# Kernel tuning notes

Measured on AMD Instinct MI355X. Metric: run time of the kernel, lower is better.

## Reference

```python
import jax, jax.numpy as jnp
import numpy as np

IN_DIM = 512
QK_DIM = IN_DIM // 8

def setup_inputs() -> dict:
    key = jax.random.key(0)
    ks = jax.random.split(key, 8)
    x = jax.random.normal(ks[0], (8, IN_DIM, 64, 64), dtype=jnp.float32)
    s_in = 1.0 / np.sqrt(IN_DIM)
    Wq = jax.random.normal(ks[1], (QK_DIM, IN_DIM), dtype=jnp.float32) * s_in
    bq = jnp.zeros((QK_DIM,), dtype=jnp.float32)
    Wk = jax.random.normal(ks[2], (QK_DIM, IN_DIM), dtype=jnp.float32) * s_in
    bk = jnp.zeros((QK_DIM,), dtype=jnp.float32)
    Wv = jax.random.normal(ks[3], (IN_DIM, IN_DIM), dtype=jnp.float32) * s_in
    bv = jnp.zeros((IN_DIM,), dtype=jnp.float32)
    # gamma initialized to zero in the module; use small nonzero so output depends on attention path
    gamma = jnp.array([0.1], dtype=jnp.float32)
    return {"x": x, "Wq": Wq, "bq": bq, "Wk": Wk, "bk": bk, "Wv": Wv, "bv": bv, "gamma": gamma}

def reference(x, Wq, bq, Wk, bk, Wv, bv, gamma):
    b, c, h, w = x.shape
    n = h * w
    xf = x.reshape(b, c, n)  # (b, C, N)
    # 1x1 convs are per-pixel linear maps over channels
    q = jnp.einsum('oc,bcn->bno', Wq, xf) + bq  # (b, N, Cq)
    k = jnp.einsum('oc,bcn->bon', Wk, xf) + bk[None, :, None]  # (b, Cq, N)
    energy = jnp.einsum('bno,bom->bnm', q, k)  # (b, N, N), no scaling (as in source)
    attention = jax.nn.softmax(energy, axis=-1)
    v = jnp.einsum('oc,bcn->bon', Wv, xf) + bv[None, :, None]  # (b, C, N)
    # out[b,c,i] = sum_j v[b,c,j] * attention[b,i,j]  (bmm with attention^T)
    out = jnp.einsum('bcj,bij->bci', v, attention).reshape(b, c, h, w)
    return gamma[0] * out + x
```

## Files before the change

### kernel.cpp

```cpp
#include <hip/hip_runtime.h>
#include <hip/hip_bf16.h>
#include <cstddef>

#define BB 8
#define CC 512
#define NN 4096
#define CQ 64
#define MQ 64
#define NJ 64

typedef short bf16x8 __attribute__((ext_vector_type(8)));
typedef float f32x4  __attribute__((ext_vector_type(4)));

static __device__ __forceinline__ unsigned bf16_bits(float f){
  unsigned u = __float_as_uint(f);
  u += 0x7fffu + ((u >> 16) & 1u);
  return u >> 16;
}
static __device__ __forceinline__ unsigned pack2bf(float lo, float hi){
  return bf16_bits(lo) | (bf16_bits(hi) << 16);
}

__global__ __launch_bounds__(256) void cvt_w_kernel(
    const float* __restrict__ Wq, const float* __restrict__ Wk,
    const float* __restrict__ Wv,
    short* __restrict__ Wqkbf, short* __restrict__ Wvbf){
  const int i = blockIdx.x*256 + threadIdx.x;
  if (i < CQ*CC){
    Wqkbf[i]         = (short)bf16_bits(Wq[i]);
    Wqkbf[CQ*CC + i] = (short)bf16_bits(Wk[i]);
  }
  Wvbf[i] = (short)bf16_bits(Wv[i]);
}

__global__ __launch_bounds__(256) void cvt_x_kernel(
    const float* __restrict__ x, short* __restrict__ xT){
  __shared__ float lds[64*67];
  const int tid = threadIdx.x;
  const int n0 = blockIdx.x*64, c0 = blockIdx.y*64, b = blockIdx.z;
  const int nl = tid & 63, cw = tid >> 6;
  const float* xp = x + ((size_t)b*CC + c0)*NN + n0;
#pragma unroll
  for (int i=0;i<16;++i){
    const int cl = cw*16 + i;
    lds[nl*67 + cl] = xp[(size_t)cl*NN + nl];
  }
  __syncthreads();
  short* xTp = xT + ((size_t)b*NN + n0)*CC + c0;
#pragma unroll
  for (int p=0;p<2;++p){
    const int nl2 = (tid>>3) + p*32;
    const int c8 = (tid&7)*8;
    const float* r = &lds[nl2*67 + c8];
    uint4 v;
    v.x = pack2bf(r[0], r[1]);
    v.y = pack2bf(r[2], r[3]);
    v.z = pack2bf(r[4], r[5]);
    v.w = pack2bf(r[6], r[7]);
    *(uint4*)&xTp[(size_t)nl2*CC + c8] = v;
  }
}

__global__ __launch_bounds__(256) void proj_qk_mfma(
    const short* __restrict__ xT, const short* __restrict__ Wqkbf,
    const float* __restrict__ bq, const float* __restrict__ bk,
    short* __restrict__ Qbf, short* __restrict__ Kbf){
  const int tid  = threadIdx.x;
  const int lane = tid & 63;
  const int w    = tid >> 6;
  const int iq   = lane & 15;
  const int q    = lane >> 4;
  const int b    = blockIdx.z;
  const int n0w  = blockIdx.x*128 + w*32;

  f32x4 acc[2][8];
#pragma unroll
  for (int ns=0;ns<2;++ns)
#pragma unroll
    for (int os=0;os<8;++os) acc[ns][os] = (f32x4){0.f,0.f,0.f,0.f};

  const short* Abase = xT + ((size_t)b*NN + n0w + iq)*CC + q*8;
  const short* Bbase = Wqkbf + (size_t)iq*CC + q*8;

  for (int ks=0; ks<16; ++ks){
    const int k = ks*32;
    bf16x8 af[2], bf[8];
#pragma unroll
    for (int ns=0;ns<2;++ns) af[ns] = *(const bf16x8*)(Abase + (size_t)ns*16*CC + k);
#pragma unroll
    for (int os=0;os<8;++os) bf[os] = *(const bf16x8*)(Bbase + (size_t)os*16*CC + k);
#pragma unroll
    for (int ns=0;ns<2;++ns)
#pragma unroll
      for (int os=0;os<8;++os)
        acc[ns][os] = __builtin_amdgcn_mfma_f32_16x16x32_bf16(af[ns], bf[os], acc[ns][os], 0,0,0);
  }
#pragma unroll
  for (int ns=0;ns<2;++ns){
#pragma unroll
    for (int os=0;os<8;++os){
      const int o = (os&4) ? ((os-4)*16 + iq) : (os*16 + iq);
      const float bias = (os<4) ? bq[o] : bk[o];
      short* dst = (os<4) ? Qbf : Kbf;
#pragma unroll
      for (int r=0;r<4;++r){
        const int n = n0w + ns*16 + q*4 + r;
        float v = acc[ns][os][r] + bias;
        if (os < 4) v *= 1.44269504088896f;
        dst[((size_t)b*NN + n)*CQ + o] = (short)bf16_bits(v);
      }
    }
  }
}

__global__ __launch_bounds__(256) void proj_v_mfma(
    const short* __restrict__ xT, const short* __restrict__ Wvbf,
    const float* __restrict__ bv, short* __restrict__ Vbf){
  const int tid  = threadIdx.x;
  const int lane = tid & 63;
  const int w    = tid >> 6;
  const int iq   = lane & 15;
  const int q    = lane >> 4;
  const int b    = blockIdx.z;
  const int c0w  = blockIdx.y*128 + (w&1)*64;
  const int n0w  = blockIdx.x*64 + (w>>1)*32;

  f32x4 acc[4][2];
#pragma unroll
  for (int cs=0;cs<4;++cs)
#pragma unroll
    for (int ns=0;ns<2;++ns) acc[cs][ns] = (f32x4){0.f,0.f,0.f,0.f};

  const short* Abase = Wvbf + (size_t)(c0w + iq)*CC + q*8;
  const short* Bbase = xT + ((size_t)b*NN + n0w + iq)*CC + q*8;

  for (int ks=0; ks<16; ++ks){
    const int k = ks*32;
    bf16x8 af[4], bf[2];
#pragma unroll
    for (int cs=0;cs<4;++cs) af[cs] = *(const bf16x8*)(Abase + (size_t)cs*16*CC + k);
#pragma unroll
    for (int ns=0;ns<2;++ns) bf[ns] = *(const bf16x8*)(Bbase + (size_t)ns*16*CC + k);
#pragma unroll
    for (int cs=0;cs<4;++cs)
#pragma unroll
      for (int ns=0;ns<2;++ns)
        acc[cs][ns] = __builtin_amdgcn_mfma_f32_16x16x32_bf16(af[cs], bf[ns], acc[cs][ns], 0,0,0);
  }
#pragma unroll
  for (int cs=0;cs<4;++cs){
#pragma unroll
    for (int r=0;r<4;++r){
      const int c = c0w + cs*16 + q*4 + r;
      const float bias = bv[c];
#pragma unroll
      for (int ns=0;ns<2;++ns){
        const int n = n0w + ns*16 + iq;
        Vbf[((size_t)b*CC + c)*NN + n] = (short)bf16_bits(acc[cs][ns][r] + bias);
      }
    }
  }
}

__global__ __launch_bounds__(256, 2) void attn_mfma_kernel(
    const short* __restrict__ Qbf, const short* __restrict__ Kbf,
    const short* __restrict__ Vbf, const float* __restrict__ x,
    const float* __restrict__ gamma, float* __restrict__ out){
  __shared__ unsigned plds[2][2048];
  __shared__ float lsum[4][MQ];

  const int tid  = threadIdx.x;
  const int lane = tid & 63;
  const int w    = tid >> 6;
  const int iq   = lane & 15;
  const int q    = lane >> 4;
  const int bid  = blockIdx.x;
  const int b    = bid & 7;
  const int ch   = ((bid >> 3) & 1) * 256;
  const int i0   = (bid >> 4) * MQ;

  bf16x8 qb[4][2];
#pragma unroll
  for (int s=0;s<4;++s){
    const short* qp = Qbf + ((size_t)b*NN + i0 + s*16 + iq)*CQ + q*8;
    qb[s][0] = *(const bf16x8*)qp;
    qb[s][1] = *(const bf16x8*)(qp + 32);
  }

  f32x4 acc[4][4];
#pragma unroll
  for (int cs=0;cs<4;++cs)
#pragma unroll
    for (int s=0;s<4;++s) acc[cs][s] = (f32x4){0.f,0.f,0.f,0.f};
  float lpart[4] = {0.f,0.f,0.f,0.f};

  const short* Kbase = Kbf + ((size_t)b*NN + w*16 + iq)*CQ + q*8;
  const short* Vbase = Vbf + ((size_t)b*CC + ch + w*64 + iq)*NN + q*8;

  const int woff  = (w*2 + (q>>1))*256 + iq*4 + (q&1)*2;
  const int roff0 = q*256 + iq*4;

  bf16x8 ka0 = *(const bf16x8*)Kbase;
  bf16x8 ka1 = *(const bf16x8*)(Kbase + 32);
  bf16x8 vc[4][2];
#pragma unroll
  for (int cs=0;cs<4;++cs){
    const short* vrow = Vbase + (size_t)cs*16*NN;
    vc[cs][0] = *(const bf16x8*)vrow;
    vc[cs][1] = *(const bf16x8*)(vrow + 32);
  }

#pragma unroll 2
  for (int jt=0; jt<NN/NJ; ++jt){
    const int buf = jt & 1;
    const int j0 = jt*NJ;

    bf16x8 vn[4][2];
    const short* vp = Vbase + j0 + NJ;
#pragma unroll
    for (int cs=0;cs<4;++cs){
      const short* vrow = vp + (size_t)cs*16*NN;
      vn[cs][0] = *(const bf16x8*)vrow;
      vn[cs][1] = *(const bf16x8*)(vrow + 32);
    }
    const short* kp = Kbase + (size_t)(j0 + NJ)*CQ;
    bf16x8 kn0 = *(const bf16x8*)kp;
    bf16x8 kn1 = *(const bf16x8*)(kp + 32);

    f32x4 sf[4];
#pragma unroll
    for (int s=0;s<4;++s){
      sf[s] = __builtin_amdgcn_mfma_f32_16x16x32_bf16(ka0, qb[s][0], (f32x4){0.f,0.f,0.f,0.f}, 0,0,0);
      sf[s] = __builtin_amdgcn_mfma_f32_16x16x32_bf16(ka1, qb[s][1], sf[s], 0,0,0);
    }
#pragma unroll
    for (int s=0;s<4;++s){
      const float p0 = __builtin_amdgcn_exp2f(sf[s][0]);
      const float p1 = __builtin_amdgcn_exp2f(sf[s][1]);
      const float p2 = __builtin_amdgcn_exp2f(sf[s][2]);
      const float p3 = __builtin_amdgcn_exp2f(sf[s][3]);
      lpart[s] += (p0+p1) + (p2+p3);
      uint2 pw;
      pw.x = pack2bf(p0, p1);
      pw.y = pack2bf(p2, p3);
      *(uint2*)&plds[buf][woff + s*64] = pw;
    }
    __builtin_amdgcn_s_waitcnt(0xc07f);
    __builtin_amdgcn_s_barrier();

#pragma unroll
    for (int s=0;s<4;++s){
      const bf16x8 pb0 = *(const bf16x8*)&plds[buf][roff0 + s*64];
      const bf16x8 pb1 = *(const bf16x8*)&plds[buf][roff0 + s*64 + 1024];
#pragma unroll
      for (int cs=0;cs<4;++cs){
        acc[cs][s] = __builtin_amdgcn_mfma_f32_16x16x32_bf16(vc[cs][0], pb0, acc[cs][s], 0,0,0);
        acc[cs][s] = __builtin_amdgcn_mfma_f32_16x16x32_bf16(vc[cs][1], pb1, acc[cs][s], 0,0,0);
      }
    }
    ka0 = kn0; ka1 = kn1;
#pragma unroll
    for (int cs=0;cs<4;++cs){
      vc[cs][0] = vn[cs][0];
      vc[cs][1] = vn[cs][1];
    }
  }

#pragma unroll
  for (int s=0;s<4;++s){
    lpart[s] += __shfl_xor(lpart[s], 16, 64);
    lpart[s] += __shfl_xor(lpart[s], 32, 64);
  }
  __syncthreads();
  if (q == 0){
#pragma unroll
    for (int s=0;s<4;++s) lsum[w][s*16 + iq] = lpart[s];
  }
  __syncthreads();
  float linv[4];
#pragma unroll
  for (int s=0;s<4;++s){
    const int i = s*16 + iq;
    linv[s] = 1.0f / (lsum[0][i] + lsum[1][i] + lsum[2][i] + lsum[3][i]);
  }

  const float gam = gamma[0];
#pragma unroll
  for (int cs=0;cs<4;++cs){
#pragma unroll
    for (int s=0;s<4;++s){
      const int cb = ch + w*64 + cs*16 + q*4;
      const int i  = i0 + s*16 + iq;
#pragma unroll
      for (int r=0;r<4;++r){
        const size_t idx = ((size_t)b*CC + cb + r)*NN + i;
        out[idx] = fmaf(gam, acc[cs][s][r]*linv[s], x[idx]);
      }
    }
  }
}

extern "C" void kernel_launch(void* const* d_in, const int* in_sizes, int n_in,
                              void* d_out, int out_size, void* d_ws, size_t ws_size,
                              hipStream_t stream){
  const float* x     = (const float*)d_in[0];
  const float* Wq    = (const float*)d_in[1];
  const float* bq    = (const float*)d_in[2];
  const float* Wk    = (const float*)d_in[3];
  const float* bk    = (const float*)d_in[4];
  const float* Wv    = (const float*)d_in[5];
  const float* bv    = (const float*)d_in[6];
  const float* gamma = (const float*)d_in[7];
  float* out = (float*)d_out;

  short* xTbf = (short*)d_ws;
  short* Qbf  = xTbf + (size_t)BB*NN*CC;
  short* Kbf  = Qbf  + (size_t)BB*NN*CQ;
  short* Vbf  = Kbf  + (size_t)BB*NN*CQ;
  short* Wqkbf= Vbf  + (size_t)BB*CC*NN;
  short* Wvbf = Wqkbf + (size_t)2*CQ*CC;

  cvt_w_kernel<<<dim3(CC*CC/256), 256, 0, stream>>>(Wq, Wk, Wv, Wqkbf, Wvbf);
  cvt_x_kernel<<<dim3(NN/64, CC/64, BB), 256, 0, stream>>>(x, xTbf);
  proj_qk_mfma<<<dim3(NN/128, 1, BB), 256, 0, stream>>>(xTbf, Wqkbf, bq, bk, Qbf, Kbf);
  proj_v_mfma<<<dim3(NN/64, CC/128, BB), 256, 0, stream>>>(xTbf, Wvbf, bv, Vbf);
  attn_mfma_kernel<<<dim3(BB*NN*2/MQ), 256, 0, stream>>>(Qbf, Kbf, Vbf, x, gamma, out);
}
```

Measured before the change: 531.3 us.

## Drop V register prefetch, raise occupancy to 3 blocks, add MFMA priority hints

The attention loop no longer keeps a full next-tile copy of V in registers. It now loads the current tile's V in two halves, one before and one after the QK MFMAs, and prefetches K just after the QK MFMAs. Launch bounds are raised from 2 to 3 blocks per CU, and s_setprio wraps the MFMA phases. The aim is to cut VGPR pressure so more waves can hide latency. The cost is that global load latency is now exposed within each iteration, which the extra occupancy has to cover.

```diff
diff --git a/kernel.cpp b/kernel.cpp
--- a/kernel.cpp
+++ b/kernel.cpp
@@ -162,7 +162,7 @@
   }
 }
 
-__global__ __launch_bounds__(256, 2) void attn_mfma_kernel(
+__global__ __launch_bounds__(256, 3) void attn_mfma_kernel(
     const short* __restrict__ Qbf, const short* __restrict__ Kbf,
     const short* __restrict__ Vbf, const float* __restrict__ x,
     const float* __restrict__ gamma, float* __restrict__ out){
@@ -202,37 +202,42 @@
 
   bf16x8 ka0 = *(const bf16x8*)Kbase;
   bf16x8 ka1 = *(const bf16x8*)(Kbase + 32);
-  bf16x8 vc[4][2];
-#pragma unroll
-  for (int cs=0;cs<4;++cs){
-    const short* vrow = Vbase + (size_t)cs*16*NN;
-    vc[cs][0] = *(const bf16x8*)vrow;
-    vc[cs][1] = *(const bf16x8*)(vrow + 32);
-  }
 
 #pragma unroll 2
   for (int jt=0; jt<NN/NJ; ++jt){
     const int buf = jt & 1;
     const int j0 = jt*NJ;
 
-    bf16x8 vn[4][2];
-    const short* vp = Vbase + j0 + NJ;
-#pragma unroll
-    for (int cs=0;cs<4;++cs){
+    bf16x8 va[4][2];
+    const short* vp = Vbase + j0;
+#pragma unroll
+    for (int cs=0;cs<2;++cs){
       const short* vrow = vp + (size_t)cs*16*NN;
-      vn[cs][0] = *(const bf16x8*)vrow;
-      vn[cs][1] = *(const bf16x8*)(vrow + 32);
-    }
-    const short* kp = Kbase + (size_t)(j0 + NJ)*CQ;
-    bf16x8 kn0 = *(const bf16x8*)kp;
-    bf16x8 kn1 = *(const bf16x8*)(kp + 32);
+      va[cs][0] = *(const bf16x8*)vrow;
+      va[cs][1] = *(const bf16x8*)(vrow + 32);
+    }
 
     f32x4 sf[4];
+    __builtin_amdgcn_s_setprio(1);
 #pragma unroll
     for (int s=0;s<4;++s){
       sf[s] = __builtin_amdgcn_mfma_f32_16x16x32_bf16(ka0, qb[s][0], (f32x4){0.f,0.f,0.f,0.f}, 0,0,0);
       sf[s] = __builtin_amdgcn_mfma_f32_16x16x32_bf16(ka1, qb[s][1], sf[s], 0,0,0);
     }
+    __builtin_amdgcn_s_setprio(0);
+
+    {
+      const short* kp = Kbase + (size_t)(j0 + NJ)*CQ;
+      ka0 = *(const bf16x8*)kp;
+      ka1 = *(const bf16x8*)(kp + 32);
+    }
+#pragma unroll
+    for (int cs=2;cs<4;++cs){
+      const short* vrow = vp + (size_t)cs*16*NN;
+      va[cs][0] = *(const bf16x8*)vrow;
+      va[cs][1] = *(const bf16x8*)(vrow + 32);
+    }
+
 #pragma unroll
     for (int s=0;s<4;++s){
       const float p0 = __builtin_amdgcn_exp2f(sf[s][0]);
@@ -248,22 +253,18 @@
     __builtin_amdgcn_s_waitcnt(0xc07f);
     __builtin_amdgcn_s_barrier();
 
+    __builtin_amdgcn_s_setprio(1);
 #pragma unroll
     for (int s=0;s<4;++s){
       const bf16x8 pb0 = *(const bf16x8*)&plds[buf][roff0 + s*64];
       const bf16x8 pb1 = *(const bf16x8*)&plds[buf][roff0 + s*64 + 1024];
 #pragma unroll
       for (int cs=0;cs<4;++cs){
-        acc[cs][s] = __builtin_amdgcn_mfma_f32_16x16x32_bf16(vc[cs][0], pb0, acc[cs][s], 0,0,0);
-        acc[cs][s] = __builtin_amdgcn_mfma_f32_16x16x32_bf16(vc[cs][1], pb1, acc[cs][s], 0,0,0);
+        acc[cs][s] = __builtin_amdgcn_mfma_f32_16x16x32_bf16(va[cs][0], pb0, acc[cs][s], 0,0,0);
+        acc[cs][s] = __builtin_amdgcn_mfma_f32_16x16x32_bf16(va[cs][1], pb1, acc[cs][s], 0,0,0);
       }
     }
-    ka0 = kn0; ka1 = kn1;
-#pragma unroll
-    for (int cs=0;cs<4;++cs){
-      vc[cs][0] = vn[cs][0];
-      vc[cs][1] = vn[cs][1];
-    }
+    __builtin_amdgcn_s_setprio(0);
   }
 
 #pragma unroll
```

Result: slower. 687.8 us (+29.5%).
